# Optimization experiments

Measured on AMD Instinct MI355X. Metric: run time of the kernel, lower is better.

Reference implementation:

```python
import jax, jax.numpy as jnp
import numpy as np

EPS = 1e-5
NUM_GROUPS = 32
N_HEADS = 8


def layer_norm(x, g, b):
    mu = jnp.mean(x, axis=-1, keepdims=True)
    var = jnp.var(x, axis=-1, keepdims=True)
    return (x - mu) * jax.lax.rsqrt(var + EPS) * g + b


def group_norm(x, g, b):
    # x: [B, C, H, W]
    B, C, H, W = x.shape
    xg = x.reshape(B, NUM_GROUPS, C // NUM_GROUPS, H, W)
    mu = jnp.mean(xg, axis=(2, 3, 4), keepdims=True)
    var = jnp.var(xg, axis=(2, 3, 4), keepdims=True)
    xn = ((xg - mu) * jax.lax.rsqrt(var + EPS)).reshape(B, C, H, W)
    return xn * g[None, :, None, None] + b[None, :, None, None]


def attention(x, ctx, wq, wk, wv, wo, bo):
    # x: [B, N, D], ctx: [B, M, Dc]
    B, N, _ = x.shape
    q = x @ wq
    k = ctx @ wk
    v = ctx @ wv
    D = q.shape[-1]
    d = D // N_HEADS
    q = q.reshape(B, N, N_HEADS, d)
    k = k.reshape(B, -1, N_HEADS, d)
    v = v.reshape(B, -1, N_HEADS, d)
    sim = jnp.einsum('bihd,bjhd->bhij', q, k) * (d ** -0.5)
    attn = jax.nn.softmax(sim, axis=-1)
    out = jnp.einsum('bhij,bjhd->bihd', attn, v).reshape(B, N, D)
    return out @ wo + bo


def reference(x, context, gn_g, gn_b, proj_in_w, proj_in_b,
              ln1_g, ln1_b, q1_w, k1_w, v1_w, o1_w, o1_b,
              ln2_g, ln2_b, q2_w, k2_w, v2_w, o2_w, o2_b,
              ln3_g, ln3_b, ff1_w, ff1_b, ff2_w, ff2_b,
              proj_out_w, proj_out_b):
    B, C, H, W = x.shape
    x_in = x
    h = group_norm(x, gn_g, gn_b)
    # 1x1 conv == channel matmul
    h = jnp.einsum('bchw,cd->bhwd', h, proj_in_w) + proj_in_b
    h = h.reshape(B, H * W, -1)  # [B, N, D]
    # BasicTransformerBlock (depth=1)
    h = attention(layer_norm(h, ln1_g, ln1_b), layer_norm(h, ln1_g, ln1_b),
                  q1_w, k1_w, v1_w, o1_w, o1_b) + h
    h = attention(layer_norm(h, ln2_g, ln2_b), context,
                  q2_w, k2_w, v2_w, o2_w, o2_b) + h
    hn = layer_norm(h, ln3_g, ln3_b)
    ff = jax.nn.gelu(hn @ ff1_w + ff1_b, approximate=False) @ ff2_w + ff2_b
    h = ff + h
    h = h.reshape(B, H, W, -1)
    out = jnp.einsum('bhwd,dc->bchw', h, proj_out_w) + proj_out_b[None, :, None, None]
    return out + x_in


def setup_inputs() -> dict:
    key = jax.random.key(0)
    ks = jax.random.split(key, 16)
    B, C, H, W = 8, 512, 32, 32
    D, Dc, L = 512, 768, 77
    s = 0.02

    def rn(k, shape):
        return jax.random.normal(k, shape, jnp.float32) * s

    return dict(
        x=jax.random.normal(ks[0], (B, C, H, W), jnp.float32),
        context=jax.random.normal(ks[1], (B, L, Dc), jnp.float32),
        gn_g=jnp.ones(C, jnp.float32), gn_b=jnp.zeros(C, jnp.float32),
        proj_in_w=rn(ks[2], (C, D)), proj_in_b=jnp.zeros(D, jnp.float32),
        ln1_g=jnp.ones(D, jnp.float32), ln1_b=jnp.zeros(D, jnp.float32),
        q1_w=rn(ks[3], (D, D)), k1_w=rn(ks[4], (D, D)), v1_w=rn(ks[5], (D, D)),
        o1_w=rn(ks[6], (D, D)), o1_b=jnp.zeros(D, jnp.float32),
        ln2_g=jnp.ones(D, jnp.float32), ln2_b=jnp.zeros(D, jnp.float32),
        q2_w=rn(ks[7], (D, D)), k2_w=rn(ks[8], (Dc, D)), v2_w=rn(ks[9], (Dc, D)),
        o2_w=rn(ks[10], (D, D)), o2_b=jnp.zeros(D, jnp.float32),
        ln3_g=jnp.ones(D, jnp.float32), ln3_b=jnp.zeros(D, jnp.float32),
        ff1_w=rn(ks[11], (D, 4 * D)), ff1_b=jnp.zeros(4 * D, jnp.float32),
        ff2_w=rn(ks[12], (4 * D, D)), ff2_b=jnp.zeros(D, jnp.float32),
        proj_out_w=rn(ks[13], (D, C)), proj_out_b=jnp.zeros(C, jnp.float32),
    )
```

## Files before the change

kernel.cpp:

```cpp
#include <hip/hip_runtime.h>

typedef unsigned short u16;
typedef unsigned int   u32;
typedef __bf16 bf16x8 __attribute__((ext_vector_type(8)));
typedef float  f32x4  __attribute__((ext_vector_type(4)));
typedef u16    u16x4  __attribute__((ext_vector_type(4)));

__device__ __forceinline__ float bf2f(u16 u) {
    union { u32 i; float f; } v; v.i = (u32)u << 16; return v.f;
}
__device__ __forceinline__ u16 f2bf(float f) {
    union { float f; u32 u; } v; v.f = f;
    u32 r = v.u + 0x7fffu + ((v.u >> 16) & 1u);
    return (u16)(r >> 16);
}
__device__ __forceinline__ float ldn(const void* p, size_t i, u32 f) {
    return f ? bf2f(((const u16*)p)[i]) : ((const float*)p)[i];
}
__device__ __forceinline__ u32 dtf(const void* gref) {
    return (((const u32*)gref)[0] == 0x3F803F80u) ? 1u : 0u;
}
__device__ __forceinline__ void async16(const void* g, void* l) {
    __builtin_amdgcn_global_load_lds(
        (__attribute__((address_space(1))) u32*)g,
        (__attribute__((address_space(3))) u32*)l, 16, 0, 0);
}
__device__ __forceinline__ float fast_erf(float x) {
    float ax = fabsf(x);
    float t = __frcp_rn(1.f + 0.3275911f * ax);
    float p = t * (0.254829592f + t * (-0.284496736f + t * (1.421413741f +
              t * (-1.453152027f + t * 1.061405429f))));
    float r = 1.f - p * __expf(-ax * ax);
    return copysignf(r, x);
}

struct TrTab {
    const void* in[12];
    u16* out[12];
    int K[12]; int N[12]; int blk0[13];
};

__global__ __launch_bounds__(256)
void prep_k(TrTab tab, int trN,
            const void* __restrict__ ctx, u16* __restrict__ ctxb, int cvtB,
            const void* __restrict__ X, const void* __restrict__ G,
            const void* __restrict__ Bt, u16* __restrict__ gout)
{
    const u32 f = dtf(G);
    const int blk = blockIdx.x;
    const int t = threadIdx.x;

    if (blk < 256) {
        __shared__ float gtile[16][264];
        __shared__ float red[8];
        __shared__ float gsh[16], bsh[16];
        const int b = blk >> 5, g = blk & 31;
        const int c0 = g * 16;
        const size_t xbase = ((size_t)b * 512 + c0) * 1024;
        if (t < 16) { gsh[t] = ldn(G, c0 + t, f); bsh[t] = ldn(Bt, c0 + t, f); }
        float s = 0.f, sq = 0.f;
        if (f) {
            for (int i = 0; i < 8; ++i) {
                union { uint4 v; u16 u[8]; } ld;
                ld.v = *(const uint4*)((const u16*)X + xbase + i * 2048 + t * 8);
#pragma unroll
                for (int j = 0; j < 8; ++j) { float v = bf2f(ld.u[j]); s += v; sq += v * v; }
            }
        } else {
            for (int i = 0; i < 16; ++i) {
                float4 v4 = *(const float4*)((const float*)X + xbase + i * 1024 + t * 4);
                s += v4.x + v4.y + v4.z + v4.w;
                sq += v4.x * v4.x + v4.y * v4.y + v4.z * v4.z + v4.w * v4.w;
            }
        }
        for (int off = 32; off; off >>= 1) { s += __shfl_xor(s, off); sq += __shfl_xor(sq, off); }
        const int w = t >> 6, lane = t & 63;
        if (lane == 0) { red[w] = s; red[4 + w] = sq; }
        __syncthreads();
        s  = red[0] + red[1] + red[2] + red[3];
        sq = red[4] + red[5] + red[6] + red[7];
        const float mean = s * (1.f / 16384.f);
        const float rstd = rsqrtf(sq * (1.f / 16384.f) - mean * mean + 1e-5f);
        for (int ch = 0; ch < 4; ++ch) {
            const int hw0 = ch * 256;
            __syncthreads();
#pragma unroll
            for (int k = 0; k < 4; ++k) {
                int slot = k * 256 + t;
                int row = slot >> 6, col = (slot & 63) * 4;
                float4 v4;
                if (f) {
                    union { uint2 v; u16 u[4]; } ld;
                    ld.v = *(const uint2*)((const u16*)X + xbase + (size_t)row * 1024 + hw0 + col);
                    v4.x = bf2f(ld.u[0]); v4.y = bf2f(ld.u[1]);
                    v4.z = bf2f(ld.u[2]); v4.w = bf2f(ld.u[3]);
                } else {
                    v4 = *(const float4*)((const float*)X + xbase + (size_t)row * 1024 + hw0 + col);
                }
                *(float4*)(&gtile[row][col]) = v4;
            }
            __syncthreads();
#pragma unroll
            for (int k = 0; k < 2; ++k) {
                int slot = k * 256 + t;
                int hwl = slot >> 1, ci0 = (slot & 1) * 8;
                union { uint4 v; u16 u[8]; } st;
#pragma unroll
                for (int j = 0; j < 8; ++j) {
                    float v = gtile[ci0 + j][hwl];
                    st.u[j] = f2bf((v - mean) * rstd * gsh[ci0 + j] + bsh[ci0 + j]);
                }
                *(uint4*)(&gout[((size_t)b * 1024 + hw0 + hwl) * 512 + c0 + ci0]) = st.v;
            }
        }
        return;
    }
    const int blk2 = blk - 256;
    if (blk2 < trN) {
        __shared__ u16 tile[32][33];
        int i = 0;
        while (i < 11 && blk2 >= tab.blk0[i + 1]) ++i;
        const void* In = tab.in[i];
        u16* Out = tab.out[i];
        const int K = tab.K[i], N = tab.N[i];
        const int lb = blk2 - tab.blk0[i];
        const int nx = N >> 5;
        const int n0 = (lb % nx) * 32, k0 = (lb / nx) * 32;
        const int tx = t & 31, ty = t >> 5;
#pragma unroll
        for (int s = 0; s < 32; s += 8)
            tile[ty + s][tx] = f2bf(ldn(In, (size_t)(k0 + ty + s) * N + n0 + tx, f));
        __syncthreads();
#pragma unroll
        for (int s = 0; s < 32; s += 8)
            Out[(size_t)(n0 + ty + s) * K + k0 + tx] = tile[tx][ty + s];
        return;
    }
    {
        int i = ((blk2 - trN) * 256 + t) * 8;
        union { uint4 v; u16 u[8]; } st;
#pragma unroll
        for (int j = 0; j < 8; ++j) st.u[j] = f2bf(ldn(ctx, i + j, f));
        *(uint4*)(&ctxb[i]) = st.v;
    }
}

__global__ __launch_bounds__(256)
void ln_k(const u16* __restrict__ X, const void* __restrict__ G,
          const void* __restrict__ Bt, u16* __restrict__ Out,
          const void* __restrict__ fref)
{
    const u32 f = dtf(fref);
    const int t = threadIdx.x, w = t >> 6, lane = t & 63;
    const size_t row = (size_t)blockIdx.x * 4 + w;
    const int col0 = lane * 8;
    union { uint4 v; u16 u[8]; } ld, st;
    ld.v = *(const uint4*)(&X[row * 512 + col0]);
    float fv[8]; float s = 0.f, sq = 0.f;
#pragma unroll
    for (int j = 0; j < 8; ++j) { fv[j] = bf2f(ld.u[j]); s += fv[j]; sq += fv[j] * fv[j]; }
    for (int off = 32; off; off >>= 1) { s += __shfl_xor(s, off); sq += __shfl_xor(sq, off); }
    const float mean = s * (1.f / 512.f);
    const float rstd = rsqrtf(sq * (1.f / 512.f) - mean * mean + 1e-5f);
#pragma unroll
    for (int j = 0; j < 8; ++j)
        st.u[j] = f2bf((fv[j] - mean) * rstd * ldn(G, col0 + j, f) + ldn(Bt, col0 + j, f));
    *(uint4*)(&Out[row * 512 + col0]) = st.v;
}

template<int MODE, int BM, int BN, int BK>
__global__ __launch_bounds__(256, (BM == 64) ? 4 : 2)
void gemm_k(const u16* __restrict__ A, const u16* __restrict__ Wt,
            const void* __restrict__ bias, const u16* Res,
            const void* __restrict__ Xres, void* Out, u16* __restrict__ Pv,
            int M, int N, int K, int MT, int NT, const void* __restrict__ fref)
{
    const u32 f = dtf(fref);
    constexpr int MI = BM / 32;
    constexpr int NI = BN / 32;
    constexpr int KC = BK / 32;
    constexpr int CPR = BK / 8;
    constexpr int SA = (BM * BK) / 2048;
    constexpr int SB = (BN * BK) / 2048;
    constexpr u32 ABYTES = (u32)BM * BK * 2;
    constexpr u32 BBYTES = (u32)BN * BK * 2;
    __shared__ u16 As[2][BM * BK];
    __shared__ u16 Bs[2][BN * BK];
    const int t = threadIdx.x;
    const int lane = t & 63;
    const int l15 = lane & 15;
    const int quad = lane >> 4;
    const int w = t >> 6;
    const int rowbase = (w >> 1) * (BM / 2);
    const int colbase = (w & 1) * (BN / 2);

    int m_t, n_t;
    {
        const int id = blockIdx.x;
        if ((MT & 7) == 0) {
            const int low = id & 7, k = id >> 3;
            n_t = k % NT;
            m_t = ((k / NT) << 3) | low;
        } else {
            n_t = id % NT;
            m_t = id / NT;
        }
    }
    const int m0 = m_t * BM;
    const int n0 = n_t * BN;

    const int nkt = K / BK;

    const u16* gA[SA]; const u16* gB[SB]; u32 lofA[SA], lofB[SB];
#pragma unroll
    for (int s = 0; s < SA; ++s) {
        int c = t + s * 256;
        int r = c / CPR, ch = c % CPR;
        int gch = (BK == 32) ? (ch ^ ((r >> 1) & 3)) : (ch ^ (r & 7));
        int gr = m0 + r;
        if (MODE == 4) gr = gr < M ? gr : M - 1;
        gA[s] = A + (size_t)gr * K + gch * 8;
        lofA[s] = (u32)c * 16;
    }
#pragma unroll
    for (int s = 0; s < SB; ++s) {
        int c = t + s * 256;
        int r = c / CPR, ch = c % CPR;
        int gch = (BK == 32) ? (ch ^ ((r >> 1) & 3)) : (ch ^ (r & 7));
        gB[s] = Wt + (size_t)(n0 + r) * K + gch * 8;
        lofB[s] = (u32)c * 16;
    }
    char* const As0 = (char*)&As[0][0];
    char* const Bs0 = (char*)&Bs[0][0];

    auto stage = [&](int kt, int buf) {
        const int ko = kt * BK;
        const u32 ab = (u32)buf * ABYTES, bb = (u32)buf * BBYTES;
#pragma unroll
        for (int s = 0; s < SA; ++s) async16(gA[s] + ko, As0 + ab + lofA[s]);
#pragma unroll
        for (int s = 0; s < SB; ++s) async16(gB[s] + ko, Bs0 + bb + lofB[s]);
    };

    f32x4 acc[MI][NI];
#pragma unroll
    for (int i = 0; i < MI; ++i)
#pragma unroll
        for (int j = 0; j < NI; ++j)
#pragma unroll
            for (int e = 0; e < 4; ++e) acc[i][j][e] = 0.f;

    const int swz = (BK == 32) ? ((l15 >> 1) & 3) : (l15 & 7);
    const u32 abase = (u32)((rowbase + l15) * BK * 2);
    const u32 bbase = (u32)((colbase + l15) * BK * 2);
    u32 choff[KC];
#pragma unroll
    for (int ks = 0; ks < KC; ++ks) choff[ks] = (u32)(((quad + 4 * ks) ^ swz) * 16);

    stage(0, 0);
    for (int kt = 0; kt < nkt; ++kt) {
        const int buf = kt & 1;
        __syncthreads();
        if (kt + 1 < nkt) stage(kt + 1, buf ^ 1);

        const u32 ab = (u32)buf * ABYTES, bb = (u32)buf * BBYTES;
        bf16x8 af[MI][KC], bfr[NI][KC];
#pragma unroll
        for (int ks = 0; ks < KC; ++ks) {
#pragma unroll
            for (int mi = 0; mi < MI; ++mi)
                af[mi][ks] = *(const bf16x8*)(As0 + ab + abase + (u32)(mi * 16 * BK * 2) + choff[ks]);
#pragma unroll
            for (int ni = 0; ni < NI; ++ni)
                bfr[ni][ks] = *(const bf16x8*)(Bs0 + bb + bbase + (u32)(ni * 16 * BK * 2) + choff[ks]);
        }
#pragma unroll
        for (int ks = 0; ks < KC; ++ks)
#pragma unroll
            for (int mi = 0; mi < MI; ++mi)
#pragma unroll
                for (int ni = 0; ni < NI; ++ni)
                    acc[mi][ni] = __builtin_amdgcn_mfma_f32_16x16x32_bf16(af[mi][ks], bfr[ni][ks], acc[mi][ni], 0, 0, 0);
    }

#pragma unroll
    for (int mi = 0; mi < MI; ++mi) {
#pragma unroll
        for (int ni = 0; ni < NI; ++ni) {
            const int col = n0 + colbase + ni * 16 + l15;
            float bv = 0.f;
            if (MODE == 0 || MODE == 1 || MODE == 2)
                bv = bias ? ldn(bias, col, f) : 0.f;
            const int row0 = m0 + rowbase + mi * 16 + quad * 4;

            if (MODE == 2) {
                size_t o0 = ((size_t)(row0 >> 10) * 512 + col) * 1024 + (row0 & 1023);
                if (f) {
                    u16x4 st;
#pragma unroll
                    for (int r = 0; r < 4; ++r)
                        st[r] = f2bf(acc[mi][ni][r] + bv + bf2f(((const u16*)Xres)[o0 + r]));
                    *(u16x4*)((u16*)Out + o0) = st;
                } else {
                    float4 xr = *(const float4*)((const float*)Xres + o0);
                    float4 st;
                    st.x = acc[mi][ni][0] + bv + xr.x;
                    st.y = acc[mi][ni][1] + bv + xr.y;
                    st.z = acc[mi][ni][2] + bv + xr.z;
                    st.w = acc[mi][ni][3] + bv + xr.w;
                    *(float4*)((float*)Out + o0) = st;
                }
                continue;
            }
            if (MODE == 3 && col >= 1024) {
                size_t o0 = ((size_t)(row0 >> 10) * 512 + (col - 1024)) * 1024 + (row0 & 1023);
                u16x4 st;
#pragma unroll
                for (int r = 0; r < 4; ++r) st[r] = f2bf(acc[mi][ni][r]);
                *(u16x4*)(Pv + o0) = st;
                continue;
            }

#pragma unroll
            for (int r = 0; r < 4; ++r) {
                const int row = row0 + r;
                if (MODE == 4 && row >= M) continue;
                float v = acc[mi][ni][r] + bv;
                if (MODE == 1) v = 0.5f * v * (1.f + fast_erf(v * 0.70710678118654752f));
                if (MODE == 3) {
                    ((u16*)Out)[(size_t)(col >> 9) * (8192 * 512) + (size_t)row * 512 + (col & 511)] = f2bf(v);
                } else if (MODE == 4) {
                    if (col < 512) {
                        ((u16*)Out)[(size_t)row * 512 + col] = f2bf(v);
                    } else {
                        u32 b = ((u32)row * 54472u) >> 22;
                        u32 j = (u32)row - b * 77u;
                        Pv[((size_t)b * 512 + (col - 512)) * 128 + j] = f2bf(v);
                    }
                } else {
                    size_t oidx = (size_t)row * N + col;
                    if (Res) v += bf2f(Res[oidx]);
                    ((u16*)Out)[oidx] = f2bf(v);
                }
            }
        }
    }
}

template<int VS>
__global__ __launch_bounds__(256, 2)
void attn_k(const u16* __restrict__ Q, const u16* __restrict__ Kb,
            const u16* __restrict__ VbT, u16* __restrict__ O, int MK)
{
    __shared__ u16 Ks[2][64 * 64];
    __shared__ u16 Vts[2][64 * 64];
    __shared__ u16 Ps[4][16 * 72];
    const int t = threadIdx.x, lane = t & 63, w = t >> 6;
    const int l15 = lane & 15, quad = lane >> 4;
    const int id = blockIdx.x;
    const int bh = id & 63, b = bh >> 3, h = bh & 7;
    const int q0 = (id >> 6) * 64, hc0 = h * 64;
    const size_t qrow0 = (size_t)b * 1024 + q0;
    const size_t kvbase = (size_t)b * MK;
    const size_t vtbase = ((size_t)b * 512 + hc0) * VS;
    const float SC = 0.18033688011112042f;
    constexpr bool FULL = (VS == 1024);

    bf16x8 aq[2];
#pragma unroll
    for (int ks = 0; ks < 2; ++ks)
        aq[ks] = *(const bf16x8*)(&Q[(qrow0 + w * 16 + l15) * 512 + hc0 + ks * 32 + quad * 8]);

    float lsum = 0.f;
    f32x4 o_acc[4];
#pragma unroll
    for (int ni = 0; ni < 4; ++ni)
#pragma unroll
        for (int e = 0; e < 4; ++e) o_acc[ni][e] = 0.f;

    const int nkt = (MK + 63) >> 6;

    char* const Ks0 = (char*)&Ks[0][0];
    char* const Vts0 = (char*)&Vts[0][0];
    const u16* gK[2]; const u16* gV[2]; u32 lof[2];
#pragma unroll
    for (int s = 0; s < 2; ++s) {
        int c = t + s * 256;
        int r = c >> 3, ch = c & 7;
        int gch = ch ^ (r & 7);
        gK[s] = Kb + (kvbase + r) * 512 + hc0 + gch * 8;
        gV[s] = VbT + vtbase + (size_t)r * VS + gch * 8;
        lof[s] = (u32)c * 16;
    }

    auto stage = [&](int kt, int buf) {
        const u32 lb = (u32)buf * 8192;
        if (FULL) {
            const size_t kOff = (size_t)kt * 32768;
            const int vOff = kt * 64;
#pragma unroll
            for (int s = 0; s < 2; ++s) async16(gK[s] + kOff, Ks0 + lb + lof[s]);
#pragma unroll
            for (int s = 0; s < 2; ++s) async16(gV[s] + vOff, Vts0 + lb + lof[s]);
        } else {
#pragma unroll
            for (int s = 0; s < 2; ++s) {
                int c = t + s * 256;
                int r = c >> 3, ch = c & 7;
                int gch = ch ^ (r & 7);
                int j = kt * 64 + r; j = j < MK ? j : MK - 1;
                async16(Kb + (kvbase + j) * 512 + hc0 + gch * 8, Ks0 + lb + (u32)c * 16);
            }
#pragma unroll
            for (int s = 0; s < 2; ++s) {
                int c = t + s * 256;
                int r = c >> 3, ch = c & 7;
                int gch = ch ^ (r & 7);
                async16(VbT + vtbase + (size_t)r * VS + kt * 64 + gch * 8, Vts0 + lb + (u32)c * 16);
            }
        }
    };

    const int swz = l15 & 7;
    const u32 kvrd = (u32)(l15 * 128);
    u32 choffB[2];
#pragma unroll
    for (int ks = 0; ks < 2; ++ks) choffB[ks] = (u32)(((quad + 4 * ks) ^ swz) * 16);
    char* const PsW = (char*)&Ps[w][0];
    const u32 pwb = (u32)(l15 * 144 + quad * 8);
    const u32 prb = (u32)(l15 * 144 + quad * 16);

    stage(0, 0);
    for (int kt = 0; kt < nkt; ++kt) {
        const int buf = kt & 1;
        __syncthreads();
        if (kt + 1 < nkt) stage(kt + 1, buf ^ 1);
        const u32 lb = (u32)buf * 8192;

        f32x4 sa[4];
#pragma unroll
        for (int ni = 0; ni < 4; ++ni)
#pragma unroll
            for (int e = 0; e < 4; ++e) sa[ni][e] = 0.f;
#pragma unroll
        for (int ks = 0; ks < 2; ++ks)
#pragma unroll
            for (int ni = 0; ni < 4; ++ni) {
                bf16x8 bk = *(const bf16x8*)(Ks0 + lb + kvrd + (u32)(ni * 2048) + choffB[ks]);
                sa[ni] = __builtin_amdgcn_mfma_f32_16x16x32_bf16(bk, aq[ks], sa[ni], 0, 0, 0);
            }

#pragma unroll
        for (int ni = 0; ni < 4; ++ni) {
            float pv[4];
#pragma unroll
            for (int r = 0; r < 4; ++r) {
                const bool valid = FULL || (kt * 64 + ni * 16 + quad * 4 + r) < MK;
                float sv = valid ? fminf(sa[ni][r] * SC, 60.f) : -1e30f;
                pv[r] = exp2f(sv);
                lsum += pv[r];
            }
            u32 lo, hi;
            asm("v_cvt_pk_bf16_f32 %0, %1, %2" : "=v"(lo) : "v"(pv[0]), "v"(pv[1]));
            asm("v_cvt_pk_bf16_f32 %0, %1, %2" : "=v"(hi) : "v"(pv[2]), "v"(pv[3]));
            uint2 pk; pk.x = lo; pk.y = hi;
            *(uint2*)(PsW + pwb + (u32)(ni * 32)) = pk;
        }
#pragma unroll
        for (int ks = 0; ks < 2; ++ks) {
            bf16x8 ap = *(const bf16x8*)(PsW + prb + (u32)(ks * 64) - (u32)(quad * 16) + choffB[ks] * 0 + (u32)(quad * 16));
            ap = *(const bf16x8*)(PsW + (u32)(l15 * 144 + ks * 64 + quad * 16));
#pragma unroll
            for (int ni = 0; ni < 4; ++ni) {
                bf16x8 bv = *(const bf16x8*)(Vts0 + lb + kvrd + (u32)(ni * 2048) + choffB[ks]);
                o_acc[ni] = __builtin_amdgcn_mfma_f32_16x16x32_bf16(ap, bv, o_acc[ni], 0, 0, 0);
            }
        }
    }
    lsum += __shfl_xor(lsum, 16);
    lsum += __shfl_xor(lsum, 32);
    const float linv = 1.f / fmaxf(lsum, 1e-30f);
    float inv[4];
#pragma unroll
    for (int r = 0; r < 4; ++r) inv[r] = __shfl(linv, quad * 4 + r);
#pragma unroll
    for (int ni = 0; ni < 4; ++ni)
#pragma unroll
        for (int r = 0; r < 4; ++r) {
            size_t row = qrow0 + w * 16 + quad * 4 + r;
            O[row * 512 + hc0 + ni * 16 + l15] = f2bf(o_acc[ni][r] * inv[r]);
        }
}

extern "C" void kernel_launch(void* const* d_in, const int* in_sizes, int n_in,
                              void* d_out, int out_size, void* d_ws, size_t ws_size,
                              hipStream_t stream)
{
    const void* x    = d_in[0];
    const void* ctx  = d_in[1];
    const void* gn_g = d_in[2];
    const void* gn_b = d_in[3];
    const void* piw  = d_in[4];
    const void* pib  = d_in[5];
    const void* ln1g = d_in[6];
    const void* ln1b = d_in[7];
    const void* q1w  = d_in[8];
    const void* k1w  = d_in[9];
    const void* v1w  = d_in[10];
    const void* o1w  = d_in[11];
    const void* o1b  = d_in[12];
    const void* ln2g = d_in[13];
    const void* ln2b = d_in[14];
    const void* q2w  = d_in[15];
    const void* k2w  = d_in[16];
    const void* v2w  = d_in[17];
    const void* o2w  = d_in[18];
    const void* o2b  = d_in[19];
    const void* ln3g = d_in[20];
    const void* ln3b = d_in[21];
    const void* f1w  = d_in[22];
    const void* f1b  = d_in[23];
    const void* f2w  = d_in[24];
    const void* f2b  = d_in[25];
    const void* pwo  = d_in[26];
    const void* pob  = d_in[27];

    u16* ws = (u16*)d_ws;
    size_t o = 0;
    u16* WT_qkv1 = ws + o; o += (size_t)1536 * 512;
    u16* WT_kv2  = ws + o; o += (size_t)1024 * 768;
    u16* WT_pi = ws + o; o += 512 * 512;
    u16* WT_o1 = ws + o; o += 512 * 512;
    u16* WT_q2 = ws + o; o += 512 * 512;
    u16* WT_o2 = ws + o; o += 512 * 512;
    u16* WT_f1 = ws + o; o += (size_t)2048 * 512;
    u16* WT_f2 = ws + o; o += (size_t)512 * 2048;
    u16* WT_po = ws + o; o += 512 * 512;
    u16* ctxb  = ws + o; o += (size_t)616 * 768;
    u16* vbTc  = ws + o; o += (size_t)8 * 512 * 128;
    u16* hb    = ws + o; o += (size_t)8192 * 512;
    u16* t0    = ws + o; o += (size_t)8192 * 512;
    u16* qb    = ws + o; o += (size_t)8192 * 512;
    u16* kb    = ws + o; o += (size_t)8192 * 512;
    u16* ab    = ws + o; o += (size_t)8192 * 512;
    u16* vbT   = ws + o; o += (size_t)8192 * 512;
    u16* ffm   = qb;

    dim3 tb(256);

    {
        TrTab tab;
        const void* ins[12] = {q1w, k1w, v1w, k2w, v2w, piw, o1w, q2w, o2w, f1w, f2w, pwo};
        u16* outs[12] = {WT_qkv1, WT_qkv1 + (size_t)512 * 512, WT_qkv1 + (size_t)1024 * 512,
                         WT_kv2, WT_kv2 + (size_t)512 * 768,
                         WT_pi, WT_o1, WT_q2, WT_o2, WT_f1, WT_f2, WT_po};
        int Ks[12] = {512, 512, 512, 768, 768, 512, 512, 512, 512, 512, 2048, 512};
        int Ns[12] = {512, 512, 512, 512, 512, 512, 512, 512, 512, 2048, 512, 512};
        int acc0 = 0;
        for (int i = 0; i < 12; ++i) {
            tab.in[i] = ins[i]; tab.out[i] = outs[i]; tab.K[i] = Ks[i]; tab.N[i] = Ns[i];
            tab.blk0[i] = acc0; acc0 += (Ns[i] / 32) * (Ks[i] / 32);
        }
        tab.blk0[12] = acc0;
        const int cvtB = 473088 / (8 * 256);
        prep_k<<<dim3(256 + acc0 + cvtB), tb, 0, stream>>>(
            tab, acc0, ctx, ctxb, cvtB, x, gn_g, gn_b, t0);
    }

    gemm_k<0, 64, 64, 64><<<dim3(1024), tb, 0, stream>>>(t0, WT_pi, pib, nullptr, nullptr, hb, nullptr, 8192, 512, 512, 128, 8, gn_g);

    ln_k<<<dim3(2048), tb, 0, stream>>>(hb, ln1g, ln1b, t0, gn_g);
    gemm_k<3, 64, 64, 64><<<dim3(3072), tb, 0, stream>>>(t0, WT_qkv1, nullptr, nullptr, nullptr, qb, vbT, 8192, 1536, 512, 128, 24, gn_g);
    attn_k<1024><<<dim3(1024), tb, 0, stream>>>(qb, kb, vbT, ab, 1024);
    gemm_k<0, 64, 64, 64><<<dim3(1024), tb, 0, stream>>>(ab, WT_o1, o1b, hb, nullptr, hb, nullptr, 8192, 512, 512, 128, 8, gn_g);

    ln_k<<<dim3(2048), tb, 0, stream>>>(hb, ln2g, ln2b, t0, gn_g);
    gemm_k<0, 64, 64, 64><<<dim3(1024), tb, 0, stream>>>(t0, WT_q2, nullptr, nullptr, nullptr, qb, nullptr, 8192, 512, 512, 128, 8, gn_g);
    gemm_k<4, 64, 64, 64><<<dim3(160), tb, 0, stream>>>(ctxb, WT_kv2, nullptr, nullptr, nullptr, kb, vbTc, 616, 1024, 768, 10, 16, gn_g);
    attn_k<128><<<dim3(1024), tb, 0, stream>>>(qb, kb, vbTc, ab, 77);
    gemm_k<0, 64, 64, 64><<<dim3(1024), tb, 0, stream>>>(ab, WT_o2, o2b, hb, nullptr, hb, nullptr, 8192, 512, 512, 128, 8, gn_g);

    ln_k<<<dim3(2048), tb, 0, stream>>>(hb, ln3g, ln3b, t0, gn_g);
    gemm_k<1, 64, 64, 64><<<dim3(4096), tb, 0, stream>>>(t0, WT_f1, f1b, nullptr, nullptr, ffm, nullptr, 8192, 2048, 512, 128, 32, gn_g);
    gemm_k<0, 64, 64, 64><<<dim3(1024), tb, 0, stream>>>(ffm, WT_f2, f2b, hb, nullptr, hb, nullptr, 8192, 512, 2048, 128, 8, gn_g);

    gemm_k<2, 64, 64, 64><<<dim3(1024), tb, 0, stream>>>(hb, WT_po, pob, nullptr, x, d_out, nullptr, 8192, 512, 512, 128, 8, gn_g);
}
```

Measured before the change: 406.3 us.

## Process two query sub-tiles per warp in attention and fold softmax scale into Q

Each attention block now handles 128 query rows instead of 64: each warp computes two 16-row query tiles against the same staged K/V tiles, so every K and V fragment read from LDS feeds two MFMAs and global K/V traffic per query is halved. The grid shrinks from 1024 to 512 blocks. The softmax scale for self-attention is applied in the QKV GEMM epilogue, removing a multiply per score in the attention loop. In exchange it raises register and LDS use per block and halves the number of blocks, which may reduce occupancy and load balance.

```diff
diff --git a/kernel.cpp b/kernel.cpp
--- a/kernel.cpp
+++ b/kernel.cpp
@@ -328,6 +328,7 @@
                 float v = acc[mi][ni][r] + bv;
                 if (MODE == 1) v = 0.5f * v * (1.f + fast_erf(v * 0.70710678118654752f));
                 if (MODE == 3) {
+                    if (col < 512) v *= 0.18033688011112042f;
                     ((u16*)Out)[(size_t)(col >> 9) * (8192 * 512) + (size_t)row * 512 + (col & 511)] = f2bf(v);
                 } else if (MODE == 4) {
                     if (col < 512) {
@@ -354,29 +355,33 @@
 {
     __shared__ u16 Ks[2][64 * 64];
     __shared__ u16 Vts[2][64 * 64];
-    __shared__ u16 Ps[4][16 * 72];
+    __shared__ u16 Ps[4][32 * 72];
     const int t = threadIdx.x, lane = t & 63, w = t >> 6;
     const int l15 = lane & 15, quad = lane >> 4;
     const int id = blockIdx.x;
     const int bh = id & 63, b = bh >> 3, h = bh & 7;
-    const int q0 = (id >> 6) * 64, hc0 = h * 64;
+    const int q0 = (id >> 6) * 128, hc0 = h * 64;
     const size_t qrow0 = (size_t)b * 1024 + q0;
     const size_t kvbase = (size_t)b * MK;
     const size_t vtbase = ((size_t)b * 512 + hc0) * VS;
     const float SC = 0.18033688011112042f;
     constexpr bool FULL = (VS == 1024);
 
-    bf16x8 aq[2];
-#pragma unroll
-    for (int ks = 0; ks < 2; ++ks)
-        aq[ks] = *(const bf16x8*)(&Q[(qrow0 + w * 16 + l15) * 512 + hc0 + ks * 32 + quad * 8]);
-
-    float lsum = 0.f;
-    f32x4 o_acc[4];
-#pragma unroll
-    for (int ni = 0; ni < 4; ++ni)
-#pragma unroll
-        for (int e = 0; e < 4; ++e) o_acc[ni][e] = 0.f;
+    bf16x8 aq[2][2];
+#pragma unroll
+    for (int mi = 0; mi < 2; ++mi)
+#pragma unroll
+        for (int ks = 0; ks < 2; ++ks)
+            aq[mi][ks] = *(const bf16x8*)(&Q[(qrow0 + w * 32 + mi * 16 + l15) * 512 + hc0 + ks * 32 + quad * 8]);
+
+    float lsum[2] = {0.f, 0.f};
+    f32x4 o_acc[2][4];
+#pragma unroll
+    for (int mi = 0; mi < 2; ++mi)
+#pragma unroll
+        for (int ni = 0; ni < 4; ++ni)
+#pragma unroll
+            for (int e = 0; e < 4; ++e) o_acc[mi][ni][e] = 0.f;
 
     const int nkt = (MK + 63) >> 6;
 
@@ -427,8 +432,6 @@
 #pragma unroll
     for (int ks = 0; ks < 2; ++ks) choffB[ks] = (u32)(((quad + 4 * ks) ^ swz) * 16);
     char* const PsW = (char*)&Ps[w][0];
-    const u32 pwb = (u32)(l15 * 144 + quad * 8);
-    const u32 prb = (u32)(l15 * 144 + quad * 16);
 
     stage(0, 0);
     for (int kt = 0; kt < nkt; ++kt) {
@@ -437,59 +440,78 @@
         if (kt + 1 < nkt) stage(kt + 1, buf ^ 1);
         const u32 lb = (u32)buf * 8192;
 
-        f32x4 sa[4];
-#pragma unroll
-        for (int ni = 0; ni < 4; ++ni)
-#pragma unroll
-            for (int e = 0; e < 4; ++e) sa[ni][e] = 0.f;
+        f32x4 sa[2][4];
+#pragma unroll
+        for (int mi = 0; mi < 2; ++mi)
+#pragma unroll
+            for (int ni = 0; ni < 4; ++ni)
+#pragma unroll
+                for (int e = 0; e < 4; ++e) sa[mi][ni][e] = 0.f;
 #pragma unroll
         for (int ks = 0; ks < 2; ++ks)
 #pragma unroll
             for (int ni = 0; ni < 4; ++ni) {
                 bf16x8 bk = *(const bf16x8*)(Ks0 + lb + kvrd + (u32)(ni * 2048) + choffB[ks]);
-                sa[ni] = __builtin_amdgcn_mfma_f32_16x16x32_bf16(bk, aq[ks], sa[ni], 0, 0, 0);
-            }
-
-#pragma unroll
-        for (int ni = 0; ni < 4; ++ni) {
-            float pv[4];
+#pragma unroll
+                for (int mi = 0; mi < 2; ++mi)
+                    sa[mi][ni] = __builtin_amdgcn_mfma_f32_16x16x32_bf16(bk, aq[mi][ks], sa[mi][ni], 0, 0, 0);
+            }
+
+#pragma unroll
+        for (int mi = 0; mi < 2; ++mi)
+#pragma unroll
+            for (int ni = 0; ni < 4; ++ni) {
+                float pv[4];
+#pragma unroll
+                for (int r = 0; r < 4; ++r) {
+                    float sv;
+                    if (FULL) {
+                        sv = fminf(sa[mi][ni][r], 60.f);
+                    } else {
+                        const bool valid = (kt * 64 + ni * 16 + quad * 4 + r) < MK;
+                        sv = valid ? fminf(sa[mi][ni][r] * SC, 60.f) : -1e30f;
+                    }
+                    pv[r] = exp2f(sv);
+                    lsum[mi] += pv[r];
+                }
+                u32 lo, hi;
+                asm("v_cvt_pk_bf16_f32 %0, %1, %2" : "=v"(lo) : "v"(pv[0]), "v"(pv[1]));
+                asm("v_cvt_pk_bf16_f32 %0, %1, %2" : "=v"(hi) : "v"(pv[2]), "v"(pv[3]));
+                uint2 pk; pk.x = lo; pk.y = hi;
+                *(uint2*)(PsW + (u32)((mi * 16 + l15) * 144 + ni * 32 + quad * 8)) = pk;
+            }
+#pragma unroll
+        for (int ks = 0; ks < 2; ++ks) {
+#pragma unroll
+            for (int mi = 0; mi < 2; ++mi) {
+                bf16x8 ap = *(const bf16x8*)(PsW + (u32)((mi * 16 + l15) * 144 + ks * 64 + quad * 16));
+#pragma unroll
+                for (int ni = 0; ni < 4; ++ni) {
+                    bf16x8 bv = *(const bf16x8*)(Vts0 + lb + kvrd + (u32)(ni * 2048) + choffB[ks]);
+                    o_acc[mi][ni] = __builtin_amdgcn_mfma_f32_16x16x32_bf16(ap, bv, o_acc[mi][ni], 0, 0, 0);
+                }
+            }
+        }
+    }
+#pragma unroll
+    for (int mi = 0; mi < 2; ++mi) {
+        lsum[mi] += __shfl_xor(lsum[mi], 16);
+        lsum[mi] += __shfl_xor(lsum[mi], 32);
+    }
+#pragma unroll
+    for (int mi = 0; mi < 2; ++mi) {
+        const float linv = 1.f / fmaxf(lsum[mi], 1e-30f);
+        float inv[4];
+#pragma unroll
+        for (int r = 0; r < 4; ++r) inv[r] = __shfl(linv, quad * 4 + r);
+#pragma unroll
+        for (int ni = 0; ni < 4; ++ni)
 #pragma unroll
             for (int r = 0; r < 4; ++r) {
-                const bool valid = FULL || (kt * 64 + ni * 16 + quad * 4 + r) < MK;
-                float sv = valid ? fminf(sa[ni][r] * SC, 60.f) : -1e30f;
-                pv[r] = exp2f(sv);
-                lsum += pv[r];
-            }
-            u32 lo, hi;
-            asm("v_cvt_pk_bf16_f32 %0, %1, %2" : "=v"(lo) : "v"(pv[0]), "v"(pv[1]));
-            asm("v_cvt_pk_bf16_f32 %0, %1, %2" : "=v"(hi) : "v"(pv[2]), "v"(pv[3]));
-            uint2 pk; pk.x = lo; pk.y = hi;
-            *(uint2*)(PsW + pwb + (u32)(ni * 32)) = pk;
-        }
-#pragma unroll
-        for (int ks = 0; ks < 2; ++ks) {
-            bf16x8 ap = *(const bf16x8*)(PsW + prb + (u32)(ks * 64) - (u32)(quad * 16) + choffB[ks] * 0 + (u32)(quad * 16));
-            ap = *(const bf16x8*)(PsW + (u32)(l15 * 144 + ks * 64 + quad * 16));
-#pragma unroll
-            for (int ni = 0; ni < 4; ++ni) {
-                bf16x8 bv = *(const bf16x8*)(Vts0 + lb + kvrd + (u32)(ni * 2048) + choffB[ks]);
-                o_acc[ni] = __builtin_amdgcn_mfma_f32_16x16x32_bf16(ap, bv, o_acc[ni], 0, 0, 0);
-            }
-        }
-    }
-    lsum += __shfl_xor(lsum, 16);
-    lsum += __shfl_xor(lsum, 32);
-    const float linv = 1.f / fmaxf(lsum, 1e-30f);
-    float inv[4];
-#pragma unroll
-    for (int r = 0; r < 4; ++r) inv[r] = __shfl(linv, quad * 4 + r);
-#pragma unroll
-    for (int ni = 0; ni < 4; ++ni)
-#pragma unroll
-        for (int r = 0; r < 4; ++r) {
-            size_t row = qrow0 + w * 16 + quad * 4 + r;
-            O[row * 512 + hc0 + ni * 16 + l15] = f2bf(o_acc[ni][r] * inv[r]);
-        }
+                size_t row = qrow0 + w * 32 + mi * 16 + quad * 4 + r;
+                O[row * 512 + hc0 + ni * 16 + l15] = f2bf(o_acc[mi][ni][r] * inv[r]);
+            }
+    }
 }
 
 extern "C" void kernel_launch(void* const* d_in, const int* in_sizes, int n_in,
@@ -571,13 +593,13 @@
 
     ln_k<<<dim3(2048), tb, 0, stream>>>(hb, ln1g, ln1b, t0, gn_g);
     gemm_k<3, 64, 64, 64><<<dim3(3072), tb, 0, stream>>>(t0, WT_qkv1, nullptr, nullptr, nullptr, qb, vbT, 8192, 1536, 512, 128, 24, gn_g);
-    attn_k<1024><<<dim3(1024), tb, 0, stream>>>(qb, kb, vbT, ab, 1024);
+    attn_k<1024><<<dim3(512), tb, 0, stream>>>(qb, kb, vbT, ab, 1024);
     gemm_k<0, 64, 64, 64><<<dim3(1024), tb, 0, stream>>>(ab, WT_o1, o1b, hb, nullptr, hb, nullptr, 8192, 512, 512, 128, 8, gn_g);
 
     ln_k<<<dim3(2048), tb, 0, stream>>>(hb, ln2g, ln2b, t0, gn_g);
     gemm_k<0, 64, 64, 64><<<dim3(1024), tb, 0, stream>>>(t0, WT_q2, nullptr, nullptr, nullptr, qb, nullptr, 8192, 512, 512, 128, 8, gn_g);
     gemm_k<4, 64, 64, 64><<<dim3(160), tb, 0, stream>>>(ctxb, WT_kv2, nullptr, nullptr, nullptr, kb, vbTc, 616, 1024, 768, 10, 16, gn_g);
-    attn_k<128><<<dim3(1024), tb, 0, stream>>>(qb, kb, vbTc, ab, 77);
+    attn_k<128><<<dim3(512), tb, 0, stream>>>(qb, kb, vbTc, ab, 77);
     gemm_k<0, 64, 64, 64><<<dim3(1024), tb, 0, stream>>>(ab, WT_o2, o2b, hb, nullptr, hb, nullptr, 8192, 512, 512, 128, 8, gn_g);
 
     ln_k<<<dim3(2048), tb, 0, stream>>>(hb, ln3g, ln3b, t0, gn_g);
```

New measurement: 399.1 us. Within noise of the previous version (-1.8%).
